# Performance work log

Hardware: AMD Instinct MI355X
Metric: run time of the kernel (lower is better)

Reference implementation:

```python
import jax, jax.numpy as jnp
import numpy as np
import math

TAU = 1.0  # value of the tau buffer (clamped min 0.001 in torch; 1.0 > that)


def setup_inputs() -> dict:
    key = jax.random.key(0)
    k_x, k_g, k_w, k_cb = jax.random.split(key, 4)
    B, n_in, K, E = 65536, 1024, 1024, 256
    x = jax.random.normal(k_x, (B, n_in), dtype=jnp.float32)
    # pre-sampled Gumbel(0,1) noise (torch samples this inside gumbel_softmax)
    u = jax.random.uniform(k_g, (B, K), dtype=jnp.float32, minval=1e-6, maxval=1.0 - 1e-6)
    gumbel = -jnp.log(-jnp.log(u))
    W_enc = jax.random.normal(k_w, (K, n_in), dtype=jnp.float32) / np.sqrt(n_in)
    b_enc = jnp.zeros((K,), dtype=jnp.float32)
    codebook = 0.5 * jax.random.normal(k_cb, (K, E), dtype=jnp.float32)  # init std=0.5
    return {"x": x, "gumbel": gumbel, "W_enc": W_enc, "b_enc": b_enc, "codebook": codebook}


def reference(x, gumbel, W_enc, b_enc, codebook):
    K = W_enc.shape[0]
    logits = x @ W_enc.T + b_enc                      # [B, K]
    soft = jax.nn.softmax((logits + gumbel) / TAU, axis=-1)  # gumbel-softmax, hard=False
    m = jnp.argmax(soft, axis=-1)                     # [B] int
    hard = jax.nn.one_hot(m, K, dtype=soft.dtype)     # [B, K]
    ste = soft + jax.lax.stop_gradient(hard - soft)   # straight-through
    z_q = ste @ codebook                              # [B, E]
    avg_p = soft.mean(axis=0)                         # [K]
    diversity = jnp.sum(avg_p * (jnp.log(jnp.clip(avg_p, 1e-9)) + math.log(K)))
    return (z_q, m, diversity, jnp.zeros((), dtype=z_q.dtype))
```

## Files before the change

kernel.cpp:

```cpp
#include <hip/hip_runtime.h>
#include <math.h>

#define BT 65536
#define NIN 1024
#define KK 1024
#define EE 256
#define MT 32
#define NB 256
#define NCB 4
#define KB 32
#define XS 36
#define WS 260
#define LOGK 6.9314718055994531f

__global__ __launch_bounds__(256, 2)
void vq_main(const float* __restrict__ x, const float* __restrict__ gum,
             const float* __restrict__ W, const float* __restrict__ bias,
             const float* __restrict__ cbk, float* __restrict__ out,
             float* __restrict__ gsum) {
    __shared__ float smem[XS * KB + WS * KB];
    float* xs = smem;
    float* ws = smem + XS * KB;

    const int tid = threadIdx.x;
    const int tc = tid & 31;
    const int tr = tid >> 5;
    const int row0 = blockIdx.x * MT;

    float lg[4][32];
    #pragma unroll
    for (int i = 0; i < 4; ++i)
        #pragma unroll
        for (int t = 0; t < 32; ++t) lg[i][t] = 0.f;

    const int xrow = tid >> 3;
    const int xn   = (tid & 7) << 2;

    for (int kc = 0; kc < NIN / KB; ++kc) {
        const int n0 = kc * KB;
        const float4 xv = *(const float4*)(x + (size_t)(row0 + xrow) * NIN + n0 + xn);
        xs[(xn + 0) * XS + xrow] = xv.x;
        xs[(xn + 1) * XS + xrow] = xv.y;
        xs[(xn + 2) * XS + xrow] = xv.z;
        xs[(xn + 3) * XS + xrow] = xv.w;

        #pragma unroll
        for (int cb = 0; cb < NCB; ++cb) {
            #pragma unroll
            for (int l = 0; l < 8; ++l) {
                const int flat = tid + l * 256;
                const int wn = (flat & 7) << 2;
                const int wc = flat >> 3;
                const float4 wv = *(const float4*)(W + (size_t)(cb * NB + wc) * NIN + n0 + wn);
                ws[(wn + 0) * WS + wc] = wv.x;
                ws[(wn + 1) * WS + wc] = wv.y;
                ws[(wn + 2) * WS + wc] = wv.z;
                ws[(wn + 3) * WS + wc] = wv.w;
            }
            __syncthreads();
            #pragma unroll
            for (int n = 0; n < KB; ++n) {
                const float4 a  = *(const float4*)(xs + n * XS + 4 * tr);
                const float4 b0 = *(const float4*)(ws + n * WS + 8 * tc);
                const float4 b1 = *(const float4*)(ws + n * WS + 8 * tc + 4);
                const float av[4] = {a.x, a.y, a.z, a.w};
                const float bv[8] = {b0.x, b0.y, b0.z, b0.w, b1.x, b1.y, b1.z, b1.w};
                #pragma unroll
                for (int i = 0; i < 4; ++i)
                    #pragma unroll
                    for (int j = 0; j < 8; ++j)
                        lg[i][cb * 8 + j] = fmaf(av[i], bv[j], lg[i][cb * 8 + j]);
            }
            __syncthreads();
        }
    }

    #pragma unroll
    for (int cb = 0; cb < NCB; ++cb) {
        const int cbase = cb * NB + 8 * tc;
        const float4 bb0 = *(const float4*)(bias + cbase);
        const float4 bb1 = *(const float4*)(bias + cbase + 4);
        #pragma unroll
        for (int i = 0; i < 4; ++i) {
            const int row = row0 + 4 * tr + i;
            const float4 g0 = *(const float4*)(gum + (size_t)row * KK + cbase);
            const float4 g1 = *(const float4*)(gum + (size_t)row * KK + cbase + 4);
            lg[i][cb * 8 + 0] += bb0.x + g0.x;
            lg[i][cb * 8 + 1] += bb0.y + g0.y;
            lg[i][cb * 8 + 2] += bb0.z + g0.z;
            lg[i][cb * 8 + 3] += bb0.w + g0.w;
            lg[i][cb * 8 + 4] += bb1.x + g1.x;
            lg[i][cb * 8 + 5] += bb1.y + g1.y;
            lg[i][cb * 8 + 6] += bb1.z + g1.z;
            lg[i][cb * 8 + 7] += bb1.w + g1.w;
        }
    }

    #pragma unroll
    for (int i = 0; i < 4; ++i) {
        float mv = -1e30f; int mi = 0;
        #pragma unroll
        for (int t = 0; t < 32; ++t) {
            const int c = (t >> 3) * NB + 8 * tc + (t & 7);
            if (lg[i][t] > mv) { mv = lg[i][t]; mi = c; }
        }
        #pragma unroll
        for (int off = 1; off < 32; off <<= 1) {
            const float ov = __shfl_xor(mv, off);
            const int   oi = __shfl_xor(mi, off);
            if (ov > mv || (ov == mv && oi < mi)) { mv = ov; mi = oi; }
        }
        float s = 0.f;
        #pragma unroll
        for (int t = 0; t < 32; ++t) {
            const float e = __expf(lg[i][t] - mv);
            lg[i][t] = e;
            s += e;
        }
        #pragma unroll
        for (int off = 1; off < 32; off <<= 1) s += __shfl_xor(s, off);
        const float rinv = 1.f / s;
        #pragma unroll
        for (int t = 0; t < 32; ++t) lg[i][t] *= rinv;

        const int row = row0 + 4 * tr + i;
        const float4 c0 = *(const float4*)(cbk + (size_t)mi * EE + 8 * tc);
        const float4 c1 = *(const float4*)(cbk + (size_t)mi * EE + 8 * tc + 4);
        *(float4*)(out + (size_t)row * EE + 8 * tc)     = c0;
        *(float4*)(out + (size_t)row * EE + 8 * tc + 4) = c1;
        if (tc == 0) out[(size_t)BT * EE + row] = (float)mi;
    }

    #pragma unroll
    for (int t = 0; t < 32; ++t) lg[0][t] += lg[1][t] + lg[2][t] + lg[3][t];
    __syncthreads();
    float* aggp = smem;
    for (int q = tid; q < KK; q += 256) aggp[q] = 0.f;
    __syncthreads();
    #pragma unroll
    for (int t = 0; t < 32; ++t)
        atomicAdd(&aggp[(t >> 3) * NB + 8 * tc + (t & 7)], lg[0][t]);
    __syncthreads();
    for (int q = tid; q < KK; q += 256) atomicAdd(&gsum[q], aggp[q]);
}

__global__ void vq_fin(const float* __restrict__ gsum, float* __restrict__ out) {
    __shared__ float red[4];
    const int tid = threadIdx.x;
    float local = 0.f;
    for (int q = tid; q < KK; q += 256) {
        const float a = gsum[q] * (1.0f / (float)BT);
        local += a * (logf(fmaxf(a, 1e-9f)) + LOGK);
    }
    #pragma unroll
    for (int off = 1; off < 64; off <<= 1) local += __shfl_xor(local, off);
    if ((tid & 63) == 0) red[tid >> 6] = local;
    __syncthreads();
    if (tid == 0) {
        out[(size_t)BT * EE + BT]     = red[0] + red[1] + red[2] + red[3];
        out[(size_t)BT * EE + BT + 1] = 0.f;
    }
}

extern "C" void kernel_launch(void* const* d_in, const int* in_sizes, int n_in,
                              void* d_out, int out_size, void* d_ws, size_t ws_size,
                              hipStream_t stream) {
    const float* x   = (const float*)d_in[0];
    const float* g   = (const float*)d_in[1];
    const float* W   = (const float*)d_in[2];
    const float* b   = (const float*)d_in[3];
    const float* cbk = (const float*)d_in[4];
    float* out  = (float*)d_out;
    float* gsum = (float*)d_ws;

    hipMemsetAsync(gsum, 0, KK * sizeof(float), stream);
    vq_main<<<BT / MT, 256, 0, stream>>>(x, g, W, b, cbk, out, gsum);
    vq_fin<<<1, 256, 0, stream>>>(gsum, out);
}
```

Baseline: 2.526 ms.

## Prefetch W/x tiles into registers and use XOR-swizzled LDS layout

Global loads of the next W and x tiles are now issued into registers before the FMA loop over the current tile, so global latency overlaps with compute. The padded LDS layout is replaced by an unpadded XOR-swizzled layout meant to avoid bank conflicts on both stores and float4 reads. Each thread's column mapping changes from 8 contiguous columns to two groups of 4 columns 128 apart, and the epilogue index math is updated to match. The prefetch adds 36 live registers per thread on top of the 128 accumulators, which risks spills or lower occupancy under launch_bounds(256,2).

```diff
diff --git a/kernel.cpp b/kernel.cpp
--- a/kernel.cpp
+++ b/kernel.cpp
@@ -9,8 +9,6 @@
 #define NB 256
 #define NCB 4
 #define KB 32
-#define XS 36
-#define WS 260
 #define LOGK 6.9314718055994531f
 
 __global__ __launch_bounds__(256, 2)
@@ -18,58 +16,82 @@
              const float* __restrict__ W, const float* __restrict__ bias,
              const float* __restrict__ cbk, float* __restrict__ out,
              float* __restrict__ gsum) {
-    __shared__ float smem[XS * KB + WS * KB];
-    float* xs = smem;
-    float* ws = smem + XS * KB;
+    __shared__ float smem[KB * NB + KB * MT];
+    float* ws = smem;
+    float* xs = smem + KB * NB;
 
     const int tid = threadIdx.x;
     const int tc = tid & 31;
     const int tr = tid >> 5;
     const int row0 = blockIdx.x * MT;
 
+    const int d    = tid & 7;
+    const int srow = tid >> 3;
+    const int wn   = d << 2;
+
+    const int xbase = wn * MT + 4 * ((srow >> 2) ^ d) + (srow & 3);
+    const int wbase = wn * NB + 4 * ((tid >> 5) ^ d) + ((tid >> 3) & 3);
+
     float lg[4][32];
     #pragma unroll
     for (int i = 0; i < 4; ++i)
         #pragma unroll
         for (int t = 0; t < 32; ++t) lg[i][t] = 0.f;
 
-    const int xrow = tid >> 3;
-    const int xn   = (tid & 7) << 2;
+    const float* xp = x + (size_t)(row0 + srow) * NIN + wn;
+    float4 xv = *(const float4*)xp;
+    float4 wv[8];
+    #pragma unroll
+    for (int l = 0; l < 8; ++l)
+        wv[l] = *(const float4*)(W + (size_t)(l * 32 + srow) * NIN + wn);
 
     for (int kc = 0; kc < NIN / KB; ++kc) {
-        const int n0 = kc * KB;
-        const float4 xv = *(const float4*)(x + (size_t)(row0 + xrow) * NIN + n0 + xn);
-        xs[(xn + 0) * XS + xrow] = xv.x;
-        xs[(xn + 1) * XS + xrow] = xv.y;
-        xs[(xn + 2) * XS + xrow] = xv.z;
-        xs[(xn + 3) * XS + xrow] = xv.w;
-
         #pragma unroll
         for (int cb = 0; cb < NCB; ++cb) {
+            if (cb == 0) {
+                xs[xbase + 0 * MT] = xv.x;
+                xs[xbase + 1 * MT] = xv.y;
+                xs[xbase + 2 * MT] = xv.z;
+                xs[xbase + 3 * MT] = xv.w;
+            }
             #pragma unroll
             for (int l = 0; l < 8; ++l) {
-                const int flat = tid + l * 256;
-                const int wn = (flat & 7) << 2;
-                const int wc = flat >> 3;
-                const float4 wv = *(const float4*)(W + (size_t)(cb * NB + wc) * NIN + n0 + wn);
-                ws[(wn + 0) * WS + wc] = wv.x;
-                ws[(wn + 1) * WS + wc] = wv.y;
-                ws[(wn + 2) * WS + wc] = wv.z;
-                ws[(wn + 3) * WS + wc] = wv.w;
+                ws[wbase + l * 32 + 0 * NB] = wv[l].x;
+                ws[wbase + l * 32 + 1 * NB] = wv[l].y;
+                ws[wbase + l * 32 + 2 * NB] = wv[l].z;
+                ws[wbase + l * 32 + 3 * NB] = wv[l].w;
             }
             __syncthreads();
-            #pragma unroll
-            for (int n = 0; n < KB; ++n) {
-                const float4 a  = *(const float4*)(xs + n * XS + 4 * tr);
-                const float4 b0 = *(const float4*)(ws + n * WS + 8 * tc);
-                const float4 b1 = *(const float4*)(ws + n * WS + 8 * tc + 4);
-                const float av[4] = {a.x, a.y, a.z, a.w};
-                const float bv[8] = {b0.x, b0.y, b0.z, b0.w, b1.x, b1.y, b1.z, b1.w};
+
+            if (cb < NCB - 1) {
                 #pragma unroll
-                for (int i = 0; i < 4; ++i)
+                for (int l = 0; l < 8; ++l)
+                    wv[l] = *(const float4*)(W + (size_t)((cb + 1) * NB + l * 32 + srow) * NIN
+                                             + kc * KB + wn);
+            } else {
+                const int nkc = (kc + 1) & (NIN / KB - 1);
+                #pragma unroll
+                for (int l = 0; l < 8; ++l)
+                    wv[l] = *(const float4*)(W + (size_t)(l * 32 + srow) * NIN + nkc * KB + wn);
+                xv = *(const float4*)(xp + nkc * KB);
+            }
+
+            for (int g = 0; g < 8; ++g) {
+                const int xo = g * 128 + 4 * (tr ^ g);
+                const int wo = g * 1024 + 4 * (tc ^ g);
+                #pragma unroll
+                for (int q = 0; q < 4; ++q) {
+                    const float4 a  = *(const float4*)(xs + xo + q * MT);
+                    const float4 b0 = *(const float4*)(ws + wo + q * NB);
+                    const float4 b1 = *(const float4*)(ws + wo + q * NB + 128);
+                    const float av[4] = {a.x, a.y, a.z, a.w};
+                    const float bv[8] = {b0.x, b0.y, b0.z, b0.w, b1.x, b1.y, b1.z, b1.w};
                     #pragma unroll
-                    for (int j = 0; j < 8; ++j)
-                        lg[i][cb * 8 + j] = fmaf(av[i], bv[j], lg[i][cb * 8 + j]);
+                    for (int i = 0; i < 4; ++i)
+                        #pragma unroll
+                        for (int j = 0; j < 8; ++j)
+                            lg[i][cb * 8 + j] = fmaf(av[i], bv[j], lg[i][cb * 8 + j]);
+                }
             }
             __syncthreads();
         }
@@ -77,14 +99,14 @@
 
     #pragma unroll
     for (int cb = 0; cb < NCB; ++cb) {
-        const int cbase = cb * NB + 8 * tc;
+        const int cbase = cb * NB + 4 * tc;
         const float4 bb0 = *(const float4*)(bias + cbase);
-        const float4 bb1 = *(const float4*)(bias + cbase + 4);
+        const float4 bb1 = *(const float4*)(bias + cbase + 128);
         #pragma unroll
         for (int i = 0; i < 4; ++i) {
             const int row = row0 + 4 * tr + i;
             const float4 g0 = *(const float4*)(gum + (size_t)row * KK + cbase);
-            const float4 g1 = *(const float4*)(gum + (size_t)row * KK + cbase + 4);
+            const float4 g1 = *(const float4*)(gum + (size_t)row * KK + cbase + 128);
             lg[i][cb * 8 + 0] += bb0.x + g0.x;
             lg[i][cb * 8 + 1] += bb0.y + g0.y;
             lg[i][cb * 8 + 2] += bb0.z + g0.z;
@@ -101,7 +123,7 @@
         float mv = -1e30f; int mi = 0;
         #pragma unroll
         for (int t = 0; t < 32; ++t) {
-            const int c = (t >> 3) * NB + 8 * tc + (t & 7);
+            const int c = (t >> 3) * NB + ((t >> 2) & 1) * 128 + 4 * tc + (t & 3);
             if (lg[i][t] > mv) { mv = lg[i][t]; mi = c; }
         }
         #pragma unroll
@@ -124,10 +146,10 @@
         for (int t = 0; t < 32; ++t) lg[i][t] *= rinv;
 
         const int row = row0 + 4 * tr + i;
-        const float4 c0 = *(const float4*)(cbk + (size_t)mi * EE + 8 * tc);
-        const float4 c1 = *(const float4*)(cbk + (size_t)mi * EE + 8 * tc + 4);
-        *(float4*)(out + (size_t)row * EE + 8 * tc)     = c0;
-        *(float4*)(out + (size_t)row * EE + 8 * tc + 4) = c1;
+        const float4 c0 = *(const float4*)(cbk + (size_t)mi * EE + 4 * tc);
+        const float4 c1 = *(const float4*)(cbk + (size_t)mi * EE + 4 * tc + 128);
+        *(float4*)(out + (size_t)row * EE + 4 * tc)       = c0;
+        *(float4*)(out + (size_t)row * EE + 4 * tc + 128) = c1;
         if (tc == 0) out[(size_t)BT * EE + row] = (float)mi;
     }
 
@@ -138,8 +160,10 @@
     for (int q = tid; q < KK; q += 256) aggp[q] = 0.f;
     __syncthreads();
     #pragma unroll
-    for (int t = 0; t < 32; ++t)
-        atomicAdd(&aggp[(t >> 3) * NB + 8 * tc + (t & 7)], lg[0][t]);
+    for (int t = 0; t < 32; ++t) {
+        const int c = (t >> 3) * NB + ((t >> 2) & 1) * 128 + 4 * tc + (t & 3);
+        atomicAdd(&aggp[c], lg[0][t]);
+    }
     __syncthreads();
     for (int q = tid; q < KK; q += 256) atomicAdd(&gsum[q], aggp[q]);
 }
```

Result: slower. 9.250 ms (+266.2%).
